# Kernel optimization log

Hardware: AMD Instinct MI355X
Metric: run time of the kernel (lower is better)

Reference implementation:

```python
import jax, jax.numpy as jnp
import numpy as np

NUM_TARGETS = 2
N_ITER = 20
REF_MIC = 1          # 1-based reference mic
CONTRAST = 'laplace'
GAMMA = 1.0
PROJ_BACK = 'mdp'
TOL = 1e-5
EPS_R = 1e-10
REG = 1e-6


def contrast_weights(r, func, gamma, eps_r):
    # phi(r) = g'(r) / r for the chosen contrast function
    r = jnp.maximum(r, eps_r)
    if func == 'laplace':
        return 1.0 / (2.0 * r)
    if func == 'gaussian':
        return jnp.ones_like(r)
    if func == 'power':
        return gamma * r ** (gamma - 2.0)
    raise ValueError(func)


def _iva_forward(X):
    M, T, F, _ = X.shape
    K = NUM_TARGETS
    # (M,T,F,2) real/imag -> complex (F,M,T)
    X_c = jnp.transpose(X[..., 0] + 1j * X[..., 1], (2, 0, 1))
    cdtype = X_c.dtype
    eyeM = jnp.eye(M, dtype=cdtype)
    W_hat = jnp.tile(eyeM[None], (F, 1, 1))
    W_hat = W_hat.at[:, K:, K:].set(-jnp.eye(M - K, dtype=cdtype))
    # input covariance (constant over iterations): (F,M,M)
    C = jnp.einsum('fmt,fnt->fmn', X_c, X_c.conj()) / T
    reg_eye = REG * eyeM  # broadcasts over F / (K,F)
    eps = jnp.finfo(jnp.float32).eps
    done = jnp.array(False)

    for _ in range(N_ITER):
        W_old = W_hat
        # current target estimates: (F,K,T)
        Y = jnp.einsum('fkm,fmt->fkt', W_hat[:, :K, :], X_c)
        r = jnp.sqrt(jnp.maximum((jnp.abs(Y) ** 2).sum(axis=0), EPS_R))  # (K,T)
        w_t = contrast_weights(r, CONTRAST, GAMMA, EPS_R).astype(cdtype)
        # weighted covariances: (K,F,M,M)
        V = jnp.einsum('kt,fmt,fnt->kfmn', w_t, X_c, X_c.conj()) / T
        V_reg = V + reg_eye

        Wn = W_hat
        for k in range(K):
            temp = Wn @ V_reg[k]                              # (F,M,M)
            e_k = jnp.zeros((F, M), dtype=cdtype).at[:, k].set(1.0)
            w_vec = jnp.linalg.solve(temp, e_k[..., None])[..., 0]  # (F,M)
            denom = jnp.sqrt(
                jnp.einsum('fm,fmn,fn->f', w_vec.conj(), V_reg[k], w_vec).real + EPS_R
            )
            Wn = Wn.at[:, k, :].set((w_vec / denom[:, None]).conj())
        # background block: J = solve(tmp[:, :, :K], tmp[:, :, K:])^H
        tmp = Wn[:, :K, :] @ C                                # (F,K,M)
        J = jnp.conj(jnp.swapaxes(jnp.linalg.solve(tmp[:, :, :K], tmp[:, :, K:]), 1, 2))
        Wn = Wn.at[:, K:, :K].set(J)

        rel = jnp.linalg.norm(Wn - W_old) / jnp.maximum(jnp.linalg.norm(W_old), eps)
        W_hat = jnp.where(done, W_old, Wn)  # freeze once converged (mimics break)
        done = done | (rel < TOL)

    W = W_hat[:, :K, :]
    Y = jnp.einsum('fkm,fmt->fkt', W, X_c)  # (F,K,T)
    if REF_MIC is not None and 0 < REF_MIC <= M:
        if PROJ_BACK == 'mdp':
            A = jnp.linalg.pinv(W)               # (F,M,K)
            scale = A[:, REF_MIC - 1, :]         # (F,K)
            Y = scale[:, :, None] * Y
        elif PROJ_BACK == 'scale_constraint':
            Wp = jnp.linalg.pinv(W)
            d = jnp.max(jnp.abs(Wp), axis=1)     # (F,K)
            Y = d[:, :, None].astype(cdtype) * Y
    Y_out = jnp.transpose(Y, (1, 2, 0))          # (K,T,F)
    return jnp.stack([Y_out.real, Y_out.imag], axis=-1)


def setup_inputs() -> dict:
    key = jax.random.key(0)
    X = jax.random.normal(key, (8, 2048, 513, 2), dtype=jnp.float32)
    return {"X": X}


def reference(X):
    return _iva_forward(X)
```

## Files before the change

### kernel.cpp

```cpp
#include <hip/hip_runtime.h>

#define F_ 513
#define M_ 8
#define T_ 2048
#define K_ 2
#define NITER 20
#define REGC 1e-6
#define EPSR 1e-10
#define TOLC 1e-5
#define NG 32
#define UPB ((F_ + 3) / 4)

typedef double2 cd;
__device__ __forceinline__ cd cmk(double r, double i){ cd z; z.x=r; z.y=i; return z; }
__device__ __forceinline__ cd cadd(cd a, cd b){ return cmk(a.x+b.x, a.y+b.y); }
__device__ __forceinline__ cd csub(cd a, cd b){ return cmk(a.x-b.x, a.y-b.y); }
__device__ __forceinline__ cd cmul(cd a, cd b){ return cmk(a.x*b.x - a.y*b.y, a.x*b.y + a.y*b.x); }
__device__ __forceinline__ cd cconj(cd a){ return cmk(a.x, -a.y); }
__device__ __forceinline__ cd cdiv(cd a, cd b){
  double d = b.x*b.x + b.y*b.y;
  return cmk((a.x*b.x + a.y*b.y)/d, (a.y*b.x - a.x*b.y)/d);
}
__device__ __forceinline__ double cabs2(cd a){ return a.x*a.x + a.y*a.y; }
__device__ __forceinline__ cd shflc(cd v, int l){
  cd r; r.x = __shfl(v.x, l, 64); r.y = __shfl(v.y, l, 64); return r;
}
__device__ __forceinline__ cd sel8(const cd x[8], int idx){
  cd r = x[0];
  #pragma unroll
  for (int q=1;q<8;++q) if (idx==q) r = x[q];
  return r;
}

__global__ __launch_bounds__(256) void pack_kernel(const float2* __restrict__ Xin, float2* __restrict__ Xc){
  __shared__ float tr[64][65];
  __shared__ float ti[64][65];
  int f0 = blockIdx.x*64, t0 = blockIdx.y*64, m = blockIdx.z;
  for (int i = threadIdx.x; i < 64*64; i += 256){
    int tl = i >> 6, fl = i & 63;
    int f = f0 + fl;
    float2 v; v.x = 0.f; v.y = 0.f;
    if (f < F_) v = Xin[((size_t)m*T_ + (t0 + tl))*F_ + f];
    tr[tl][fl] = v.x; ti[tl][fl] = v.y;
  }
  __syncthreads();
  for (int i = threadIdx.x; i < 64*64; i += 256){
    int fl = i >> 6, tl = i & 63;
    int f = f0 + fl;
    if (f < F_){
      float2 v; v.x = tr[tl][fl]; v.y = ti[tl][fl];
      Xc[((size_t)f*8 + m)*T_ + (t0 + tl)] = v;
    }
  }
}

__global__ __launch_bounds__(256) void winit_kernel(float2* __restrict__ W){
  int idx = blockIdx.x*256 + threadIdx.x;
  if (idx >= F_*64) return;
  int l = idx & 63; int i = l>>3, j = l&7;
  float v = (i==j) ? (i < K_ ? 1.f : -1.f) : 0.f;
  float2 o; o.x = v; o.y = 0.f;
  W[idx] = o;
}

__device__ const int PMt[36] = {0,0,0,0,0,0,0,0,1,1,1,1,1,1,1,2,2,2,2,2,2,3,3,3,3,3,4,4,4,4,5,5,5,6,6,7};
__device__ const int PNt[36] = {0,1,2,3,4,5,6,7,1,2,3,4,5,6,7,2,3,4,5,6,7,3,4,5,6,7,4,5,6,7,5,6,7,6,7,7};

template<int MODE>
__global__ __launch_bounds__(256) void cov_kernel(const float2* __restrict__ Xc, const float* __restrict__ wts,
                                                  cd* __restrict__ outC, const int* __restrict__ flags){
  if (MODE == 1 && *(volatile const int*)flags) return;
  __shared__ float2 xs[8][512];
  __shared__ float wsm[2][512];
  int f = blockIdx.x;
  int tid = threadIdx.x;
  int wave = tid >> 6, lane = tid & 63;
  double a0r[9], a0i[9], a1r[9], a1i[9];
  #pragma unroll
  for (int pi=0; pi<9; ++pi){ a0r[pi]=0; a0i[pi]=0; a1r[pi]=0; a1i[pi]=0; }
  for (int c=0; c<4; ++c){
    for (int idx=tid; idx<8*256; idx+=256){
      int m = idx >> 8, q = idx & 255;
      ((float4*)&xs[m][0])[q] = ((const float4*)(Xc + ((size_t)f*8 + m)*T_ + c*512))[q];
    }
    if (MODE == 1){
      for (int idx=tid; idx<256; idx+=256){
        int k = idx >> 7, q = idx & 127;
        ((float4*)&wsm[k][0])[q] = ((const float4*)(wts + k*T_ + c*512))[q];
      }
    }
    __syncthreads();
    for (int t=lane; t<512; t+=64){
      float w0=0.f, w1=0.f;
      if (MODE==1){ w0 = wsm[0][t]; w1 = wsm[1][t]; }
      #pragma unroll
      for (int pi=0; pi<9; ++pi){
        int p = wave + pi*4;
        int m = PMt[p], n = PNt[p];
        float2 av = xs[m][t], bv = xs[n][t];
        float zr = av.x*bv.x + av.y*bv.y;
        float zi = av.y*bv.x - av.x*bv.y;
        if (MODE == 0){ a0r[pi] += zr; a0i[pi] += zi; }
        else { a0r[pi] += w0*zr; a0i[pi] += w0*zi; a1r[pi] += w1*zr; a1i[pi] += w1*zi; }
      }
    }
    __syncthreads();
  }
  const double inv = 1.0 / (double)T_;
  #pragma unroll
  for (int pi=0; pi<9; ++pi){
    int p = wave + pi*4;
    int m = PMt[p], n = PNt[p];
    double r0=a0r[pi], i0=a0i[pi], r1=a1r[pi], i1=a1i[pi];
    for (int off=32; off; off>>=1){
      r0 += __shfl_down(r0, off, 64);
      i0 += __shfl_down(i0, off, 64);
      if (MODE==1){ r1 += __shfl_down(r1, off, 64); i1 += __shfl_down(i1, off, 64); }
    }
    if (lane == 0){
      if (MODE == 0){
        outC[(size_t)f*64 + m*8 + n] = cmk(r0*inv, i0*inv);
        outC[(size_t)f*64 + n*8 + m] = cmk(r0*inv, -i0*inv);
      } else {
        outC[((size_t)0*F_ + f)*64 + m*8 + n] = cmk(r0*inv, i0*inv);
        outC[((size_t)0*F_ + f)*64 + n*8 + m] = cmk(r0*inv, -i0*inv);
        outC[((size_t)1*F_ + f)*64 + m*8 + n] = cmk(r1*inv, i1*inv);
        outC[((size_t)1*F_ + f)*64 + n*8 + m] = cmk(r1*inv, -i1*inv);
      }
    }
  }
}

__global__ __launch_bounds__(256) void yr_kernel(const float2* __restrict__ Xc, const float2* __restrict__ Wg,
                                                 float* __restrict__ part, const int* __restrict__ flags){
  if (*(volatile const int*)flags) return;
  int g = blockIdx.y;
  int t = blockIdx.x*256 + threadIdx.x;
  float acc0 = 0.f, acc1 = 0.f;
  for (int f = g; f < F_; f += NG){
    const float2* Wf = Wg + (size_t)f*64;
    float2 y0; y0.x=0; y0.y=0;
    float2 y1; y1.x=0; y1.y=0;
    #pragma unroll
    for (int m=0;m<8;++m){
      float2 xv = Xc[((size_t)f*8 + m)*T_ + t];
      float2 w0 = Wf[m];
      float2 w1 = Wf[8+m];
      y0.x += w0.x*xv.x - w0.y*xv.y; y0.y += w0.x*xv.y + w0.y*xv.x;
      y1.x += w1.x*xv.x - w1.y*xv.y; y1.y += w1.x*xv.y + w1.y*xv.x;
    }
    acc0 += y0.x*y0.x + y0.y*y0.y;
    acc1 += y1.x*y1.x + y1.y*y1.y;
  }
  part[((size_t)g*2+0)*T_ + t] = acc0;
  part[((size_t)g*2+1)*T_ + t] = acc1;
}

__global__ __launch_bounds__(256) void rw_kernel(const float* __restrict__ part, float* __restrict__ wts,
                                                 const int* __restrict__ flags){
  if (*(volatile const int*)flags) return;
  int v = blockIdx.x*256 + threadIdx.x;
  int k = v >> 11, t = v & (T_-1);
  double s = 0;
  #pragma unroll
  for (int g=0; g<NG; ++g) s += (double)part[((size_t)g*2+k)*T_ + t];
  wts[v] = (float)(0.5 / sqrt(fmax(s, EPSR)));
}

__global__ __launch_bounds__(256) void update_kernel(const cd* __restrict__ Vg, const cd* __restrict__ Cg,
                                                     float2* __restrict__ Wg,
                                                     double* __restrict__ dsum, double* __restrict__ osum,
                                                     int* __restrict__ flags){
  if (*(volatile const int*)flags) return;
  int lane = threadIdx.x & 63;
  int w = threadIdx.x >> 6;
  int f = blockIdx.x*4 + w;
  int i = lane >> 3, j = lane & 7;
  double ds = 0.0, os = 0.0;
  if (f < F_){
    float2 wf = Wg[(size_t)f*64 + lane];
    cd Wn = cmk(wf.x, wf.y);
    cd Wold = Wn;
    cd x[8];
    #pragma unroll
    for (int k=0; k<K_; ++k){
      cd Vr = Vg[((size_t)k*F_ + f)*64 + lane];
      if (i == j) Vr.x += REGC;
      cd temp = cmk(0,0);
      #pragma unroll
      for (int q=0;q<8;++q) temp = cadd(temp, cmul(shflc(Wn, i*8+q), shflc(Vr, q*8+j)));
      cd b = cmk(i==k ? 1.0 : 0.0, 0.0);
      for (int p=0; p<8; ++p){
        double pv = (j==p && i>=p) ? cabs2(temp) : -1.0;
        int pidx = i;
        for (int off=32; off; off>>=1){
          double ov = __shfl_xor(pv, off, 64);
          int oi = __shfl_xor(pidx, off, 64);
          if (ov > pv){ pv = ov; pidx = oi; }
        }
        cd tp = shflc(temp, pidx*8 + j);
        cd tq = shflc(temp, p*8 + j);
        cd bp_ = shflc(b, pidx*8 + j);
        cd bq_ = shflc(b, p*8 + j);
        if (i == p){ temp = tp; b = bp_; }
        else if (i == pidx){ temp = tq; b = bq_; }
        cd tip = shflc(temp, i*8 + p);
        cd tpp = shflc(temp, p*8 + p);
        cd tpj = shflc(temp, p*8 + j);
        cd bpr = shflc(b, p*8 + j);
        cd fac = cdiv(tip, tpp);
        if (i > p){ temp = csub(temp, cmul(fac, tpj)); b = csub(b, cmul(fac, bpr)); }
      }
      #pragma unroll
      for (int p=7; p>=0; --p){
        cd s = shflc(b, p*8);
        #pragma unroll
        for (int q=p+1; q<8; ++q){
          cd tpq = shflc(temp, p*8 + q);
          s = csub(s, cmul(tpq, x[q]));
        }
        x[p] = cdiv(s, shflc(temp, p*8 + p));
      }
      cd xi = sel8(x, i), xj = sel8(x, j);
      cd z = cmul(cconj(xi), Vr);
      double dl = z.x*xj.x - z.y*xj.y;
      for (int off=32; off; off>>=1) dl += __shfl_xor(dl, off, 64);
      double denom = sqrt(dl + EPSR);
      if (i == k){ Wn = cmk(xj.x/denom, -xj.y/denom); }
    }
    cd Cc = Cg[(size_t)f*64 + lane];
    cd tmp = cmk(0,0);
    #pragma unroll
    for (int q=0;q<8;++q) tmp = cadd(tmp, cmul(shflc(Wn, i*8+q), shflc(Cc, q*8+j)));
    cd A = shflc(tmp, 0), B = shflc(tmp, 1), C2 = shflc(tmp, 8), D = shflc(tmp, 9);
    cd det = csub(cmul(A,D), cmul(B,C2));
    cd t0 = shflc(tmp, i);
    cd t1 = shflc(tmp, 8 + i);
    cd Z0 = cdiv(csub(cmul(D,t0), cmul(B,t1)), det);
    cd Z1 = cdiv(csub(cmul(A,t1), cmul(C2,t0)), det);
    if (i >= K_ && j < K_){
      cd Z = (j==0) ? Z0 : Z1;
      Wn = cconj(Z);
    }
    ds = cabs2(csub(Wn, Wold));
    os = cabs2(Wold);
    for (int off=32; off; off>>=1){
      ds += __shfl_xor(ds, off, 64);
      os += __shfl_xor(os, off, 64);
    }
    float2 wo; wo.x = (float)Wn.x; wo.y = (float)Wn.y;
    Wg[(size_t)f*64 + lane] = wo;
  }
  __shared__ double sd[4], so[4];
  __shared__ int lastFlag;
  if (lane == 0){ sd[w] = ds; so[w] = os; }
  __syncthreads();
  if (threadIdx.x == 0){
    dsum[blockIdx.x] = sd[0]+sd[1]+sd[2]+sd[3];
    osum[blockIdx.x] = so[0]+so[1]+so[2]+so[3];
  }
  __threadfence();
  if (threadIdx.x == 0){
    int tk = atomicAdd(&flags[1], 1);
    lastFlag = (tk == UPB-1) ? 1 : 0;
  }
  __syncthreads();
  if (lastFlag && threadIdx.x < 64){
    __threadfence();
    double d=0, o=0;
    for (int idx=lane; idx<UPB; idx+=64){
      d += ((volatile double*)dsum)[idx];
      o += ((volatile double*)osum)[idx];
    }
    for (int off=32; off; off>>=1){ d += __shfl_xor(d, off, 64); o += __shfl_xor(o, off, 64); }
    if (lane == 0){
      flags[1] = 0;
      double rel = sqrt(d) / fmax(sqrt(o), 1.1920928955078125e-7);
      if (rel < TOLC) flags[0] = 1;
    }
  }
}

__global__ __launch_bounds__(256) void scale_kernel(const float2* __restrict__ Wg, float2* __restrict__ scale){
  int f = blockIdx.x*256 + threadIdx.x;
  if (f >= F_) return;
  cd w0[8], w1[8];
  #pragma unroll
  for (int m=0;m<8;++m){
    float2 a = Wg[(size_t)f*64 + m];     w0[m] = cmk(a.x, a.y);
    float2 b = Wg[(size_t)f*64 + 8 + m]; w1[m] = cmk(b.x, b.y);
  }
  cd G00 = cmk(0,0), G01 = cmk(0,0), G11 = cmk(0,0);
  #pragma unroll
  for (int m=0;m<8;++m){
    G00 = cadd(G00, cmul(w0[m], cconj(w0[m])));
    G01 = cadd(G01, cmul(w0[m], cconj(w1[m])));
    G11 = cadd(G11, cmul(w1[m], cconj(w1[m])));
  }
  cd G10 = cconj(G01);
  cd det = csub(cmul(G00,G11), cmul(G01,G10));
  cd I00 = cdiv(G11, det), I01 = cdiv(cmk(-G01.x,-G01.y), det);
  cd I10 = cdiv(cmk(-G10.x,-G10.y), det), I11 = cdiv(G00, det);
  cd c0 = cconj(w0[0]), c1 = cconj(w1[0]);
  cd s0 = cadd(cmul(c0, I00), cmul(c1, I10));
  cd s1 = cadd(cmul(c0, I01), cmul(c1, I11));
  float2 o0; o0.x=(float)s0.x; o0.y=(float)s0.y;
  float2 o1; o1.x=(float)s1.x; o1.y=(float)s1.y;
  scale[(size_t)f*2 + 0] = o0;
  scale[(size_t)f*2 + 1] = o1;
}

__global__ __launch_bounds__(256) void out_kernel(const float2* __restrict__ Xc, const float2* __restrict__ Wg,
                                                  const float2* __restrict__ scale, float2* __restrict__ out){
  __shared__ float re0[32][65], im0[32][65], re1[32][65], im1[32][65];
  int f0 = blockIdx.x*32, t0 = blockIdx.y*64;
  int lane = threadIdx.x & 63, w = threadIdx.x >> 6;
  for (int fl = w; fl < 32; fl += 4){
    int f = f0 + fl;
    if (f < F_){
      const float2* Wf = Wg + (size_t)f*64;
      int t = t0 + lane;
      float2 y0; y0.x=0; y0.y=0;
      float2 y1; y1.x=0; y1.y=0;
      #pragma unroll
      for (int m=0;m<8;++m){
        float2 xv = Xc[((size_t)f*8 + m)*T_ + t];
        float2 w0 = Wf[m];
        float2 w1 = Wf[8+m];
        y0.x += w0.x*xv.x - w0.y*xv.y; y0.y += w0.x*xv.y + w0.y*xv.x;
        y1.x += w1.x*xv.x - w1.y*xv.y; y1.y += w1.x*xv.y + w1.y*xv.x;
      }
      float2 s0 = scale[(size_t)f*2 + 0];
      float2 s1 = scale[(size_t)f*2 + 1];
      re0[fl][lane] = s0.x*y0.x - s0.y*y0.y; im0[fl][lane] = s0.x*y0.y + s0.y*y0.x;
      re1[fl][lane] = s1.x*y1.x - s1.y*y1.y; im1[fl][lane] = s1.x*y1.y + s1.y*y1.x;
    }
  }
  __syncthreads();
  for (int i = threadIdx.x; i < 32*64; i += 256){
    int tl = i >> 5, fl = i & 31;
    int f = f0 + fl;
    if (f < F_){
      int t = t0 + tl;
      float2 o0; o0.x = re0[fl][tl]; o0.y = im0[fl][tl];
      float2 o1; o1.x = re1[fl][tl]; o1.y = im1[fl][tl];
      out[((size_t)(0*T_ + t))*F_ + f] = o0;
      out[((size_t)(1*T_ + t))*F_ + f] = o1;
    }
  }
}

extern "C" void kernel_launch(void* const* d_in, const int* in_sizes, int n_in,
                              void* d_out, int out_size, void* d_ws, size_t ws_size,
                              hipStream_t stream) {
  const float2* Xin = (const float2*)d_in[0];
  char* ws = (char*)d_ws;
  size_t off = 0;
  auto alloc = [&](size_t bytes) -> void* {
    void* p = ws + off;
    off += (bytes + 255) & ~(size_t)255;
    return p;
  };
  float2* Xc   = (float2*)alloc((size_t)F_*M_*T_*8);
  cd*     Cm   = (cd*)alloc((size_t)F_*64*16);
  cd*     Vm   = (cd*)alloc((size_t)K_*F_*64*16);
  float2* W    = (float2*)alloc((size_t)F_*64*8);
  float*  part = (float*)alloc((size_t)NG*K_*T_*4);
  float*  wts  = (float*)alloc((size_t)K_*T_*4);
  double* dsum = (double*)alloc((size_t)UPB*8);
  double* osum = (double*)alloc((size_t)UPB*8);
  float2* sc   = (float2*)alloc((size_t)F_*K_*8);
  int*    flags= (int*)alloc(256);
  if (off > ws_size) return;

  hipMemsetAsync(flags, 0, 8, stream);

  pack_kernel<<<dim3(9, 32, 8), 256, 0, stream>>>(Xin, Xc);
  winit_kernel<<<(F_*64 + 255)/256, 256, 0, stream>>>(W);
  cov_kernel<0><<<F_, 256, 0, stream>>>(Xc, nullptr, Cm, flags);

  for (int it=0; it<NITER; ++it){
    yr_kernel<<<dim3(T_/256, NG), 256, 0, stream>>>(Xc, W, part, flags);
    rw_kernel<<<(K_*T_ + 255)/256, 256, 0, stream>>>(part, wts, flags);
    cov_kernel<1><<<F_, 256, 0, stream>>>(Xc, wts, Vm, flags);
    update_kernel<<<UPB, 256, 0, stream>>>(Vm, Cm, W, dsum, osum, flags);
  }

  scale_kernel<<<(F_ + 255)/256, 256, 0, stream>>>(W, sc);
  out_kernel<<<dim3(17, 32), 256, 0, stream>>>(Xc, W, sc, (float2*)d_out);
}
```

Before: 2.043 ms.

## Split covariance over time slices, fuse weight reduction into cov kernel

The covariance kernel now runs a 2D grid over frequency and four time slices with 1024-thread blocks, so each wave handles fewer Hermitian pairs and more blocks run concurrently. Partial covariances per slice are summed in the update kernel. The separate contrast-weight kernel is removed: each cov block reduces the yr partials for its time slice itself, and NG is doubled for more yr parallelism. In exchange, every frequency block redundantly re-reduces the partial sums for its slice, and partial covariance storage grows.

```diff
diff --git a/kernel.cpp b/kernel.cpp
--- a/kernel.cpp
+++ b/kernel.cpp
@@ -8,7 +8,8 @@
 #define REGC 1e-6
 #define EPSR 1e-10
 #define TOLC 1e-5
-#define NG 32
+#define NG 64
+#define TS 4
 #define UPB ((F_ + 3) / 4)
 
 typedef double2 cd;
@@ -67,65 +68,75 @@
 __device__ const int PNt[36] = {0,1,2,3,4,5,6,7,1,2,3,4,5,6,7,2,3,4,5,6,7,3,4,5,6,7,4,5,6,7,5,6,7,6,7,7};
 
 template<int MODE>
-__global__ __launch_bounds__(256) void cov_kernel(const float2* __restrict__ Xc, const float* __restrict__ wts,
-                                                  cd* __restrict__ outC, const int* __restrict__ flags){
+__global__ __launch_bounds__(1024) void cov_kernel(const float2* __restrict__ Xc, const float* __restrict__ part,
+                                                   cd* __restrict__ outP, const int* __restrict__ flags){
   if (MODE == 1 && *(volatile const int*)flags) return;
   __shared__ float2 xs[8][512];
   __shared__ float wsm[2][512];
-  int f = blockIdx.x;
+  int f = blockIdx.x, s = blockIdx.y;
   int tid = threadIdx.x;
   int wave = tid >> 6, lane = tid & 63;
-  double a0r[9], a0i[9], a1r[9], a1i[9];
-  #pragma unroll
-  for (int pi=0; pi<9; ++pi){ a0r[pi]=0; a0i[pi]=0; a1r[pi]=0; a1i[pi]=0; }
-  for (int c=0; c<4; ++c){
-    for (int idx=tid; idx<8*256; idx+=256){
-      int m = idx >> 8, q = idx & 255;
-      ((float4*)&xs[m][0])[q] = ((const float4*)(Xc + ((size_t)f*8 + m)*T_ + c*512))[q];
-    }
-    if (MODE == 1){
-      for (int idx=tid; idx<256; idx+=256){
-        int k = idx >> 7, q = idx & 127;
-        ((float4*)&wsm[k][0])[q] = ((const float4*)(wts + k*T_ + c*512))[q];
-      }
-    }
-    __syncthreads();
-    for (int t=lane; t<512; t+=64){
-      float w0=0.f, w1=0.f;
-      if (MODE==1){ w0 = wsm[0][t]; w1 = wsm[1][t]; }
-      #pragma unroll
-      for (int pi=0; pi<9; ++pi){
-        int p = wave + pi*4;
-        int m = PMt[p], n = PNt[p];
-        float2 av = xs[m][t], bv = xs[n][t];
-        float zr = av.x*bv.x + av.y*bv.y;
-        float zi = av.y*bv.x - av.x*bv.y;
-        if (MODE == 0){ a0r[pi] += zr; a0i[pi] += zi; }
-        else { a0r[pi] += w0*zr; a0i[pi] += w0*zi; a1r[pi] += w1*zr; a1i[pi] += w1*zi; }
-      }
-    }
-    __syncthreads();
-  }
-  const double inv = 1.0 / (double)T_;
-  #pragma unroll
-  for (int pi=0; pi<9; ++pi){
-    int p = wave + pi*4;
-    int m = PMt[p], n = PNt[p];
-    double r0=a0r[pi], i0=a0i[pi], r1=a1r[pi], i1=a1i[pi];
+  if (MODE == 1){
+    int k = tid >> 9, t = tid & 511;
+    double sum = 0;
+    #pragma unroll 8
+    for (int g=0; g<NG; ++g) sum += (double)part[((size_t)g*2+k)*T_ + s*512 + t];
+    wsm[k][t] = (float)(0.5 / sqrt(fmax(sum, EPSR)));
+  }
+  for (int idx=tid; idx<2048; idx+=1024){
+    int m = idx >> 8, q = idx & 255;
+    ((float4*)&xs[m][0])[q] = ((const float4*)(Xc + ((size_t)f*8 + m)*T_ + s*512))[q];
+  }
+  __syncthreads();
+  int m0 = PMt[wave],    n0 = PNt[wave];
+  int m1 = PMt[wave+16], n1 = PNt[wave+16];
+  bool has2 = (wave < 4);
+  int m2 = has2 ? PMt[wave+32] : 0, n2 = has2 ? PNt[wave+32] : 0;
+  double r0[3]={0,0,0}, i0[3]={0,0,0}, r1[3]={0,0,0}, i1[3]={0,0,0};
+  #pragma unroll
+  for (int ti=0; ti<8; ++ti){
+    int t = lane + ti*64;
+    float w0=0.f, w1=0.f;
+    if (MODE==1){ w0 = wsm[0][t]; w1 = wsm[1][t]; }
+    float2 a0v = xs[m0][t], b0v = xs[n0][t];
+    float2 a1v = xs[m1][t], b1v = xs[n1][t];
+    float zr0 = a0v.x*b0v.x + a0v.y*b0v.y, zi0 = a0v.y*b0v.x - a0v.x*b0v.y;
+    float zr1 = a1v.x*b1v.x + a1v.y*b1v.y, zi1 = a1v.y*b1v.x - a1v.x*b1v.y;
+    if (MODE==0){
+      r0[0] += zr0; i0[0] += zi0;
+      r0[1] += zr1; i0[1] += zi1;
+    } else {
+      r0[0] += w0*zr0; i0[0] += w0*zi0; r1[0] += w1*zr0; i1[0] += w1*zi0;
+      r0[1] += w0*zr1; i0[1] += w0*zi1; r1[1] += w1*zr1; i1[1] += w1*zi1;
+    }
+    if (has2){
+      float2 a2v = xs[m2][t], b2v = xs[n2][t];
+      float zr2 = a2v.x*b2v.x + a2v.y*b2v.y, zi2 = a2v.y*b2v.x - a2v.x*b2v.y;
+      if (MODE==0){ r0[2] += zr2; i0[2] += zi2; }
+      else { r0[2] += w0*zr2; i0[2] += w0*zi2; r1[2] += w1*zr2; i1[2] += w1*zi2; }
+    }
+  }
+  const double inv = 1.0/(double)T_;
+  #pragma unroll
+  for (int pi=0; pi<3; ++pi){
+    int p = wave + pi*16;
+    if (p >= 36) break;
+    double a=r0[pi], b=i0[pi], c=r1[pi], d=i1[pi];
     for (int off=32; off; off>>=1){
-      r0 += __shfl_down(r0, off, 64);
-      i0 += __shfl_down(i0, off, 64);
-      if (MODE==1){ r1 += __shfl_down(r1, off, 64); i1 += __shfl_down(i1, off, 64); }
-    }
-    if (lane == 0){
-      if (MODE == 0){
-        outC[(size_t)f*64 + m*8 + n] = cmk(r0*inv, i0*inv);
-        outC[(size_t)f*64 + n*8 + m] = cmk(r0*inv, -i0*inv);
+      a += __shfl_down(a, off, 64);
+      b += __shfl_down(b, off, 64);
+      if (MODE==1){ c += __shfl_down(c, off, 64); d += __shfl_down(d, off, 64); }
+    }
+    if (lane==0){
+      int m = PMt[p], n = PNt[p];
+      if (MODE==0){
+        outP[((size_t)f*TS + s)*64 + m*8+n] = cmk(a*inv, b*inv);
+        outP[((size_t)f*TS + s)*64 + n*8+m] = cmk(a*inv, -b*inv);
       } else {
-        outC[((size_t)0*F_ + f)*64 + m*8 + n] = cmk(r0*inv, i0*inv);
-        outC[((size_t)0*F_ + f)*64 + n*8 + m] = cmk(r0*inv, -i0*inv);
-        outC[((size_t)1*F_ + f)*64 + m*8 + n] = cmk(r1*inv, i1*inv);
-        outC[((size_t)1*F_ + f)*64 + n*8 + m] = cmk(r1*inv, -i1*inv);
+        outP[(((size_t)0*F_+f)*TS + s)*64 + m*8+n] = cmk(a*inv, b*inv);
+        outP[(((size_t)0*F_+f)*TS + s)*64 + n*8+m] = cmk(a*inv, -b*inv);
+        outP[(((size_t)1*F_+f)*TS + s)*64 + m*8+n] = cmk(c*inv, d*inv);
+        outP[(((size_t)1*F_+f)*TS + s)*64 + n*8+m] = cmk(c*inv, -d*inv);
       }
     }
   }
@@ -156,18 +167,7 @@
   part[((size_t)g*2+1)*T_ + t] = acc1;
 }
 
-__global__ __launch_bounds__(256) void rw_kernel(const float* __restrict__ part, float* __restrict__ wts,
-                                                 const int* __restrict__ flags){
-  if (*(volatile const int*)flags) return;
-  int v = blockIdx.x*256 + threadIdx.x;
-  int k = v >> 11, t = v & (T_-1);
-  double s = 0;
-  #pragma unroll
-  for (int g=0; g<NG; ++g) s += (double)part[((size_t)g*2+k)*T_ + t];
-  wts[v] = (float)(0.5 / sqrt(fmax(s, EPSR)));
-}
-
-__global__ __launch_bounds__(256) void update_kernel(const cd* __restrict__ Vg, const cd* __restrict__ Cg,
+__global__ __launch_bounds__(256) void update_kernel(const cd* __restrict__ Vp, const cd* __restrict__ Cp,
                                                      float2* __restrict__ Wg,
                                                      double* __restrict__ dsum, double* __restrict__ osum,
                                                      int* __restrict__ flags){
@@ -184,7 +184,10 @@
     cd x[8];
     #pragma unroll
     for (int k=0; k<K_; ++k){
-      cd Vr = Vg[((size_t)k*F_ + f)*64 + lane];
+      cd Vr = cmk(0,0);
+      #pragma unroll
+      for (int s2=0; s2<TS; ++s2)
+        Vr = cadd(Vr, Vp[(((size_t)k*F_ + f)*TS + s2)*64 + lane]);
       if (i == j) Vr.x += REGC;
       cd temp = cmk(0,0);
       #pragma unroll
@@ -228,7 +231,10 @@
       double denom = sqrt(dl + EPSR);
       if (i == k){ Wn = cmk(xj.x/denom, -xj.y/denom); }
     }
-    cd Cc = Cg[(size_t)f*64 + lane];
+    cd Cc = cmk(0,0);
+    #pragma unroll
+    for (int s2=0; s2<TS; ++s2)
+      Cc = cadd(Cc, Cp[((size_t)f*TS + s2)*64 + lane]);
     cd tmp = cmk(0,0);
     #pragma unroll
     for (int q=0;q<8;++q) tmp = cadd(tmp, cmul(shflc(Wn, i*8+q), shflc(Cc, q*8+j)));
@@ -362,11 +368,10 @@
     return p;
   };
   float2* Xc   = (float2*)alloc((size_t)F_*M_*T_*8);
-  cd*     Cm   = (cd*)alloc((size_t)F_*64*16);
-  cd*     Vm   = (cd*)alloc((size_t)K_*F_*64*16);
+  cd*     Cp   = (cd*)alloc((size_t)F_*TS*64*16);
+  cd*     Vp   = (cd*)alloc((size_t)K_*F_*TS*64*16);
   float2* W    = (float2*)alloc((size_t)F_*64*8);
   float*  part = (float*)alloc((size_t)NG*K_*T_*4);
-  float*  wts  = (float*)alloc((size_t)K_*T_*4);
   double* dsum = (double*)alloc((size_t)UPB*8);
   double* osum = (double*)alloc((size_t)UPB*8);
   float2* sc   = (float2*)alloc((size_t)F_*K_*8);
@@ -377,13 +382,12 @@
 
   pack_kernel<<<dim3(9, 32, 8), 256, 0, stream>>>(Xin, Xc);
   winit_kernel<<<(F_*64 + 255)/256, 256, 0, stream>>>(W);
-  cov_kernel<0><<<F_, 256, 0, stream>>>(Xc, nullptr, Cm, flags);
+  cov_kernel<0><<<dim3(F_, TS), 1024, 0, stream>>>(Xc, nullptr, Cp, flags);
 
   for (int it=0; it<NITER; ++it){
     yr_kernel<<<dim3(T_/256, NG), 256, 0, stream>>>(Xc, W, part, flags);
-    rw_kernel<<<(K_*T_ + 255)/256, 256, 0, stream>>>(part, wts, flags);
-    cov_kernel<1><<<F_, 256, 0, stream>>>(Xc, wts, Vm, flags);
-    update_kernel<<<UPB, 256, 0, stream>>>(Vm, Cm, W, dsum, osum, flags);
+    cov_kernel<1><<<dim3(F_, TS), 1024, 0, stream>>>(Xc, part, Vp, flags);
+    update_kernel<<<UPB, 256, 0, stream>>>(Vp, Cp, W, dsum, osum, flags);
   }
 
   scale_kernel<<<(F_ + 255)/256, 256, 0, stream>>>(W, sc);
```

New measurement: 2.290 ms. +12.1%, slower.
